# Performance work log

Measured on AMD Instinct MI355X. Metric: run time of the kernel, lower is better.

Reference implementation:

```python
import jax, jax.numpy as jnp
import numpy as np

N_NODES = 100000
D_FEAT = 128
BATCH = 32768
K_NEIGH = 32
NUM_SAMPLE = 10


def setup_inputs() -> dict:
    key = jax.random.key(0)
    k1, k2, k3 = jax.random.split(key, 3)
    features = jax.random.normal(k1, (N_NODES, D_FEAT), dtype=jnp.float32)
    nodes = jax.random.randint(k2, (BATCH,), 0, N_NODES)
    neighs = jax.random.randint(k3, (BATCH, K_NEIGH), 0, N_NODES)
    return {"features": features, "nodes": nodes, "neighs": neighs, "num_sample": NUM_SAMPLE}


def reference(features, nodes, neighs, num_sample):
    # Gather center and candidate-neighbor features from the node table.
    center = features[nodes]            # [B, D]
    neigh_feats = features[neighs]      # [B, K, D]
    # Cosine similarity of each center to each of its K candidate neighbors
    # (matches similarity = center @ neighbors^T / (||center|| * ||neighbors||)).
    dots = jnp.einsum('bd,bkd->bk', center, neigh_feats)                 # [B, K]
    c_norm = jnp.linalg.norm(center, axis=-1, keepdims=True)             # [B, 1]
    n_norm = jnp.linalg.norm(neigh_feats, axis=-1)                       # [B, K]
    sim = dots / (c_norm * n_norm)
    # Top-num_sample neighbor selection by descending similarity
    # (replaces the per-node torch.sort + list slicing).
    _, top_idx = jax.lax.top_k(sim, num_sample)                          # [B, k]
    # Masked mean over selected neighbors (replaces the dense mask.mm(embed_matrix))
    sel = jnp.take_along_axis(neigh_feats, top_idx[..., None], axis=1)   # [B, k, D]
    to_feats = jax.nn.relu(jnp.mean(sel, axis=1))                        # [B, D]
    return to_feats
```

## Files before the change

### kernel.cpp

```cpp
#include <hip/hip_runtime.h>

#define K_NEIGH 32
#define D_FEAT  128

__device__ __forceinline__ float readlane_f(float v, int l) {
    return __int_as_float(__builtin_amdgcn_readlane(__float_as_int(v), l));
}

__global__ __launch_bounds__(256, 3) void intra_agg_kernel(
    const float* __restrict__ features,
    const int*   __restrict__ nodes,
    const int*   __restrict__ neighs,
    const int*   __restrict__ num_sample_p,
    float*       __restrict__ out,
    int batch)
{
    const int tid  = blockIdx.x * blockDim.x + threadIdx.x;
    const int lane = threadIdx.x & 63;
    int b = tid >> 6;
    if (b >= batch) return;
    b = __builtin_amdgcn_readfirstlane(b);

    const int  ns = *num_sample_p;
    const int* nb = neighs + (size_t)b * K_NEIGH;

    const int   cnode = nodes[b];
    const float2 c2 = ((const float2*)(features + (size_t)cnode * D_FEAT))[lane];

    float2 rows[K_NEIGH];
    #pragma unroll
    for (int r = 0; r < K_NEIGH; ++r) {
        const int nidx = nb[r];
        rows[r] = ((const float2*)(features + (size_t)nidx * D_FEAT))[lane];
    }

    float cc = c2.x * c2.x + c2.y * c2.y;
    #pragma unroll
    for (int m = 32; m >= 1; m >>= 1) cc += __shfl_xor(cc, m);
    const float cn = sqrtf(cc);

    float dt[K_NEIGH], n2[K_NEIGH];
    #pragma unroll
    for (int r = 0; r < K_NEIGH; ++r) {
        dt[r] = c2.x * rows[r].x + c2.y * rows[r].y;
        n2[r] = rows[r].x * rows[r].x + rows[r].y * rows[r].y;
    }

    #pragma unroll
    for (int o = 32; o >= 2; o >>= 1) {
        const bool up = (lane & o) != 0;
        #pragma unroll
        for (int r = 0; r < o / 2; ++r) {
            const float sd = up ? dt[r] : dt[r + o / 2];
            const float sn = up ? n2[r] : n2[r + o / 2];
            const float rd = __shfl_xor(sd, o);
            const float rn = __shfl_xor(sn, o);
            const float kd = up ? dt[r + o / 2] : dt[r];
            const float kn = up ? n2[r + o / 2] : n2[r];
            dt[r] = kd + rd;
            n2[r] = kn + rn;
        }
    }
    dt[0] += __shfl_xor(dt[0], 1);
    n2[0] += __shfl_xor(n2[0], 1);

    const int   myrow = lane >> 1;
    const float sim   = dt[0] / (cn * sqrtf(n2[0]));

    int rank = 0;
    #pragma unroll
    for (int j = 0; j < K_NEIGH; ++j) {
        const float sj = readlane_f(sim, 2 * j);
        rank += (sj > sim || (sj == sim && j < myrow)) ? 1 : 0;
    }

    const unsigned long long bal = __ballot(rank < ns);
    unsigned long long x = bal & 0x5555555555555555ull;
    x = (x | (x >> 1))  & 0x3333333333333333ull;
    x = (x | (x >> 2))  & 0x0F0F0F0F0F0F0F0Full;
    x = (x | (x >> 4))  & 0x00FF00FF00FF00FFull;
    x = (x | (x >> 8))  & 0x0000FFFF0000FFFFull;
    x = (x | (x >> 16)) & 0x00000000FFFFFFFFull;
    const unsigned mask = (unsigned)x;

    float2 acc = make_float2(0.f, 0.f);
    #pragma unroll
    for (int r = 0; r < K_NEIGH; ++r) {
        const float s = (float)((mask >> r) & 1u);
        acc.x = fmaf(rows[r].x, s, acc.x);
        acc.y = fmaf(rows[r].y, s, acc.y);
    }
    const float nsf = (float)ns;
    float2 ov;
    ov.x = fmaxf(acc.x / nsf, 0.f);
    ov.y = fmaxf(acc.y / nsf, 0.f);
    ((float2*)(out + (size_t)b * D_FEAT))[lane] = ov;
}

extern "C" void kernel_launch(void* const* d_in, const int* in_sizes, int n_in,
                              void* d_out, int out_size, void* d_ws, size_t ws_size,
                              hipStream_t stream) {
    const float* features = (const float*)d_in[0];
    const int*   nodes    = (const int*)d_in[1];
    const int*   neighs   = (const int*)d_in[2];
    const int*   ns       = (const int*)d_in[3];
    float*       out      = (float*)d_out;

    const int batch  = in_sizes[1];
    const int blocks = (batch + 3) / 4;

    intra_agg_kernel<<<blocks, 256, 0, stream>>>(features, nodes, neighs, ns, out, batch);
}
```

Measured before the change: 153.9 us.

## Drop register-held neighbor rows, re-gather selected rows after top-k selection

Stops keeping all 32 neighbor rows in registers. Each pair of rows is reduced on the fly with a first butterfly stage, and the mask-selected rows are read again from memory afterward with a scalar loop over the set bits. The lower register pressure lets the launch-bounds occupancy target rise from 3 to 6 waves. In exchange it issues about ten extra row gathers per batch item, which will likely hit in cache, and it uses a serial ctz loop.

```diff
diff --git a/kernel.cpp b/kernel.cpp
--- a/kernel.cpp
+++ b/kernel.cpp
@@ -7,7 +7,7 @@
     return __int_as_float(__builtin_amdgcn_readlane(__float_as_int(v), l));
 }
 
-__global__ __launch_bounds__(256, 3) void intra_agg_kernel(
+__global__ __launch_bounds__(256, 6) void intra_agg_kernel(
     const float* __restrict__ features,
     const int*   __restrict__ nodes,
     const int*   __restrict__ neighs,
@@ -27,45 +27,52 @@
     const int   cnode = nodes[b];
     const float2 c2 = ((const float2*)(features + (size_t)cnode * D_FEAT))[lane];
 
-    float2 rows[K_NEIGH];
-    #pragma unroll
-    for (int r = 0; r < K_NEIGH; ++r) {
-        const int nidx = nb[r];
-        rows[r] = ((const float2*)(features + (size_t)nidx * D_FEAT))[lane];
-    }
-
     float cc = c2.x * c2.x + c2.y * c2.y;
     #pragma unroll
     for (int m = 32; m >= 1; m >>= 1) cc += __shfl_xor(cc, m);
     const float cn = sqrtf(cc);
 
-    float dt[K_NEIGH], n2[K_NEIGH];
+    const bool hi32 = (lane & 32) != 0;
+
+    float s[16], t[16];
     #pragma unroll
-    for (int r = 0; r < K_NEIGH; ++r) {
-        dt[r] = c2.x * rows[r].x + c2.y * rows[r].y;
-        n2[r] = rows[r].x * rows[r].x + rows[r].y * rows[r].y;
+    for (int r = 0; r < 16; ++r) {
+        const int ia = nb[r];
+        const int ib = nb[r + 16];
+        const float2 va = ((const float2*)(features + (size_t)ia * D_FEAT))[lane];
+        const float2 vb = ((const float2*)(features + (size_t)ib * D_FEAT))[lane];
+        const float da  = c2.x * va.x + c2.y * va.y;
+        const float db  = c2.x * vb.x + c2.y * vb.y;
+        const float na  = va.x * va.x + va.y * va.y;
+        const float nbq = vb.x * vb.x + vb.y * vb.y;
+        const float sd = hi32 ? da : db;
+        const float sn = hi32 ? na : nbq;
+        const float rd = __shfl_xor(sd, 32);
+        const float rn = __shfl_xor(sn, 32);
+        s[r] = (hi32 ? db : da) + rd;
+        t[r] = (hi32 ? nbq : na) + rn;
     }
 
     #pragma unroll
-    for (int o = 32; o >= 2; o >>= 1) {
+    for (int o = 16; o >= 2; o >>= 1) {
         const bool up = (lane & o) != 0;
         #pragma unroll
         for (int r = 0; r < o / 2; ++r) {
-            const float sd = up ? dt[r] : dt[r + o / 2];
-            const float sn = up ? n2[r] : n2[r + o / 2];
+            const float sd = up ? s[r] : s[r + o / 2];
+            const float sn = up ? t[r] : t[r + o / 2];
             const float rd = __shfl_xor(sd, o);
             const float rn = __shfl_xor(sn, o);
-            const float kd = up ? dt[r + o / 2] : dt[r];
-            const float kn = up ? n2[r + o / 2] : n2[r];
-            dt[r] = kd + rd;
-            n2[r] = kn + rn;
+            const float kd = up ? s[r + o / 2] : s[r];
+            const float kn = up ? t[r + o / 2] : t[r];
+            s[r] = kd + rd;
+            t[r] = kn + rn;
         }
     }
-    dt[0] += __shfl_xor(dt[0], 1);
-    n2[0] += __shfl_xor(n2[0], 1);
+    s[0] += __shfl_xor(s[0], 1);
+    t[0] += __shfl_xor(t[0], 1);
 
     const int   myrow = lane >> 1;
-    const float sim   = dt[0] / (cn * sqrtf(n2[0]));
+    const float sim   = s[0] / (cn * sqrtf(t[0]));
 
     int rank = 0;
     #pragma unroll
@@ -81,14 +88,16 @@
     x = (x | (x >> 4))  & 0x00FF00FF00FF00FFull;
     x = (x | (x >> 8))  & 0x0000FFFF0000FFFFull;
     x = (x | (x >> 16)) & 0x00000000FFFFFFFFull;
-    const unsigned mask = (unsigned)x;
+    unsigned mask = (unsigned)x;
+    mask = __builtin_amdgcn_readfirstlane(mask);
 
     float2 acc = make_float2(0.f, 0.f);
-    #pragma unroll
-    for (int r = 0; r < K_NEIGH; ++r) {
-        const float s = (float)((mask >> r) & 1u);
-        acc.x = fmaf(rows[r].x, s, acc.x);
-        acc.y = fmaf(rows[r].y, s, acc.y);
+    unsigned m = mask;
+    while (m) {
+        const int r = __builtin_ctz(m); m &= m - 1;
+        const int nidx = nb[r];
+        const float2 v = ((const float2*)(features + (size_t)nidx * D_FEAT))[lane];
+        acc.x += v.x; acc.y += v.y;
     }
     const float nsf = (float)ns;
     float2 ov;
```

Result: slower. 226.0 us (+46.9%).
